# Kernel optimization log

Measured on AMD Instinct MI355X. Metric: run time of the kernel, lower is better.

## Reference

```python
import jax, jax.numpy as jnp
import numpy as np

KERNEL = 5
STRIDE = 1
DN = ('NHWC', 'HWIO', 'NHWC')
PRIOR_VAR = 0.01


def setup_inputs() -> dict:
    key = jax.random.key(0)
    k1, k2, k3 = jax.random.split(key, 3)
    mu_in = jax.random.normal(k1, (32, 224, 224, 3), dtype=jnp.float32)
    # GlorotNormal-ish scale for a 5x5x3 -> 64 kernel
    w_mu = jax.random.normal(k2, (5, 5, 3, 64), dtype=jnp.float32) * 0.12
    # original init: uniform in [min_sigma, ini_sigma] = [-4.6, -2.25]
    w_sigma = jax.random.uniform(k3, (64,), dtype=jnp.float32, minval=-4.6, maxval=-2.25)
    return {"mu_in": mu_in, "w_mu": w_mu, "w_sigma": w_sigma}


def reference(mu_in, w_mu, w_sigma):
    # KL regularizer: broadcast of (64,) logvar against (5,5,3,64) mu, mean over all
    kl = 0.5 * jnp.mean(
        jnp.log(PRIOR_VAR) - 1.0 - w_sigma
        + jax.nn.softplus(w_sigma) / PRIOR_VAR
        + jnp.square(w_mu) / PRIOR_VAR
    )

    w_sigma_2 = jax.nn.softplus(w_sigma)  # log(1+exp(w_sigma))

    # Mean path: standard conv2d, VALID, stride 1, NHWC
    mu_out = jax.lax.conv_general_dilated(
        mu_in, w_mu, (STRIDE, STRIDE), 'VALID', dimension_numbers=DN
    )  # [B, Ho, Wo, K]

    # Variance path: per-output-location sum over the k*k*C patch of x^2 / x_dim.
    # Same math as the original extract_patches + reduce_sum, but computed as a
    # channel-summed box filter on x^2 (no im2col materialization).
    C = mu_in.shape[-1]
    x_dim = jnp.asarray(KERNEL * KERNEL * C, mu_in.dtype)
    ones_k = jnp.ones((KERNEL, KERNEL, C, 1), mu_in.dtype)
    sq = jax.lax.conv_general_dilated(
        jnp.square(mu_in), ones_k, (STRIDE, STRIDE), 'VALID', dimension_numbers=DN
    ) / x_dim  # [B, Ho, Wo, 1]

    Sigma_out = jax.nn.softplus(w_sigma_2 * sq)  # broadcast -> [B, Ho, Wo, K]
    return (mu_out, Sigma_out, kl)
```

## Files before the change

### kernel.cpp

```cpp
#include <hip/hip_runtime.h>
#include <math.h>

#define BATCH 32
#define HIN   224
#define WIN   224
#define CIN   3
#define KOUT  64
#define RK    5
#define HOUT  220
#define WOUT  220

#define TS     16
#define PATCH  20
#define SROWS  24
#define NTOT ((size_t)BATCH * HOUT * WOUT * KOUT)

typedef float  v4f    __attribute__((ext_vector_type(4)));
typedef short  short8 __attribute__((ext_vector_type(8)));

#define WS_WF_FRAGS 768
#define WS_WSG_OFF  12288

__device__ __forceinline__ float exp2_hw(float x) { float r; asm("v_exp_f32 %0, %1" : "=v"(r) : "v"(x)); return r; }
__device__ __forceinline__ float log2_hw(float x) { float r; asm("v_log_f32 %0, %1" : "=v"(r) : "v"(x)); return r; }
#define LOG2E 1.44269504088896f
#define LN2   0.69314718055995f

__device__ __forceinline__ float softplus_hw(float x) {
    float t = exp2_hw(-fabsf(x) * LOG2E);
    return fmaxf(x, 0.0f) + LN2 * log2_hw(1.0f + t);
}
__device__ __forceinline__ float softplus_pos(float y) {
    return y + LN2 * log2_hw(1.0f + exp2_hw(-y * LOG2E));
}
__device__ __forceinline__ short f2bf(float x) {
    unsigned u = __float_as_uint(x);
    u = (u + 0x7FFFu + ((u >> 16) & 1u)) >> 16;
    return (short)u;
}

__global__ __launch_bounds__(256) void vdp_prep_kernel(
    const float* __restrict__ w_mu, const float* __restrict__ w_sigma, void* __restrict__ ws)
{
    short8* wf = (short8*)ws;
    float* wsg = (float*)((char*)ws + WS_WSG_OFF);
    const int t = threadIdx.x;
    for (int f = t; f < WS_WF_FRAGS; f += 256) {
        const int s  = f >> 8;
        const int nb = (f >> 6) & 3;
        const int l  = f & 63;
        const int ch = nb * 16 + (l & 15);
        const int h2 = l >> 4;
        short8 r;
        #pragma unroll
        for (int i = 0; i < 8; ++i) {
            const int k = s * 32 + h2 * 8 + i;
            const int kh = k >> 4, inner = k & 15;
            float v = 0.0f;
            if (inner < 15 && k < 80) {
                const int kw = inner / 3;
                const int c  = inner - kw * 3;
                v = w_mu[((kh * 5 + kw) * 3 + c) * KOUT + ch];
            }
            r[i] = f2bf(v);
        }
        wf[f] = r;
    }
    if (t < KOUT) wsg[t] = softplus_hw(w_sigma[t]);
}

__global__ __launch_bounds__(256, 4) void vdp_conv_kernel(
    const float* __restrict__ mu_in, const void* __restrict__ ws, float* __restrict__ out)
{
    __shared__ float s_row[SROWS][64];
    __shared__ float s_ssq[PATCH][PATCH];
    __shared__ float s_sq[TS * TS];

    const int tid  = threadIdx.x;
    const int lane = tid & 63;
    const int wid  = tid >> 6;
    const int p    = lane & 15;
    const int h2   = lane >> 4;

    const int b = blockIdx.z;
    int ho0 = blockIdx.y * TS; if (ho0 > HOUT - TS) ho0 = HOUT - TS;
    int wo0 = blockIdx.x * TS; if (wo0 > WOUT - TS) wo0 = WOUT - TS;

    const short8* wfg = (const short8*)ws;
    short8 wf[12];
    #pragma unroll
    for (int f = 0; f < 12; ++f) wf[f] = wfg[f * 64 + lane];
    const float* wsg_g = (const float*)((const char*)ws + WS_WSG_OFF);
    const v4f wsg_kg = *(const v4f*)(wsg_g + p * 4);

    for (int idx = tid; idx < SROWS * 64; idx += 256) {
        const int r = idx >> 6, c = idx & 63;
        int rg = ho0 + r; if (rg > HIN - 1) rg = HIN - 1;
        float v = 0.0f;
        if (c < 60) v = mu_in[(((size_t)b * HIN + rg) * WIN + wo0) * CIN + c];
        s_row[r][c] = v;
    }
    __syncthreads();

    for (int idx = tid; idx < PATCH * PATCH; idx += 256) {
        const int r = idx / PATCH;
        const int px = idx - r * PATCH;
        const float x0 = s_row[r][3 * px], x1 = s_row[r][3 * px + 1], x2 = s_row[r][3 * px + 2];
        s_ssq[r][px] = fmaf(x0, x0, fmaf(x1, x1, x2 * x2));
    }
    __syncthreads();

    {
        const int pr = tid >> 4, pc = tid & 15;
        float acc = 0.0f;
        #pragma unroll
        for (int kh = 0; kh < RK; ++kh)
            #pragma unroll
            for (int kw = 0; kw < RK; ++kw)
                acc += s_ssq[pr + kh][pc + kw];
        s_sq[tid] = acc * (1.0f / 75.0f);
    }
    __syncthreads();

    #pragma unroll 1
    for (int j = 0; j < 4; ++j) {
        const int rt = (wid << 2) | j;
        const size_t rowbase = (((size_t)b * HOUT + ho0 + rt) * WOUT + wo0) * KOUT;

        short8 pf[3];
        #pragma unroll
        for (int s = 0; s < 3; ++s) {
            const float* rp = &s_row[rt + 2 * s + (h2 >> 1)][3 * p + 8 * (h2 & 1)];
            short8 r;
            #pragma unroll
            for (int i = 0; i < 8; ++i) r[i] = f2bf(rp[i]);
            pf[s] = r;
        }

        v4f acc[4];
        #pragma unroll
        for (int nb = 0; nb < 4; ++nb) {
            v4f a = {0.0f, 0.0f, 0.0f, 0.0f};
            #pragma unroll
            for (int s = 0; s < 3; ++s)
                a = __builtin_amdgcn_mfma_f32_16x16x32_bf16(wf[s * 4 + nb], pf[s], a, 0, 0, 0);
            acc[nb] = a;
        }

        float* mp = out + rowbase + (size_t)p * KOUT + h2 * 4;
        #pragma unroll
        for (int nb = 0; nb < 4; ++nb)
            *(v4f*)(mp + nb * 16) = acc[nb];

        float* sp = out + NTOT + rowbase + p * 4;
        #pragma unroll
        for (int pp = 0; pp < 4; ++pp) {
            const int px = (h2 << 2) | pp;
            const float sq = s_sq[(rt << 4) | px];
            v4f sg;
            sg.x = softplus_pos(wsg_kg.x * sq);
            sg.y = softplus_pos(wsg_kg.y * sq);
            sg.z = softplus_pos(wsg_kg.z * sq);
            sg.w = softplus_pos(wsg_kg.w * sq);
            *(v4f*)(sp + (size_t)px * KOUT) = sg;
        }
    }
}

__global__ __launch_bounds__(256) void vdp_kl_kernel(
    const float* __restrict__ w_mu,
    const float* __restrict__ w_sigma,
    float* __restrict__ out)
{
    __shared__ float red[4];
    const int tid = threadIdx.x;

    float s = 0.0f;
    for (int i = tid; i < RK * RK * CIN * KOUT; i += 256) {
        const float v = w_mu[i];
        s = fmaf(v, v, s);
    }
    float u = s * (100.0f / 4800.0f);
    if (tid < KOUT) {
        const float ws = w_sigma[tid];
        u += (-ws + softplus_hw(ws) * 100.0f) * (1.0f / 64.0f);
    }
    #pragma unroll
    for (int off = 32; off > 0; off >>= 1)
        u += __shfl_down(u, off, 64);
    if ((tid & 63) == 0) red[tid >> 6] = u;
    __syncthreads();
    if (tid == 0) {
        const float U = red[0] + red[1] + red[2] + red[3];
        out[2 * NTOT] = 0.5f * (-4.6051701860f - 1.0f + U);
    }
}

extern "C" void kernel_launch(void* const* d_in, const int* in_sizes, int n_in,
                              void* d_out, int out_size, void* d_ws, size_t ws_size,
                              hipStream_t stream)
{
    (void)in_sizes; (void)n_in; (void)ws_size; (void)out_size;
    const float* mu_in   = (const float*)d_in[0];
    const float* w_mu    = (const float*)d_in[1];
    const float* w_sigma = (const float*)d_in[2];
    float* out = (float*)d_out;

    vdp_prep_kernel<<<1, 256, 0, stream>>>(w_mu, w_sigma, d_ws);
    dim3 grid((WOUT + TS - 1) / TS, (HOUT + TS - 1) / TS, BATCH);
    vdp_conv_kernel<<<grid, 256, 0, stream>>>(mu_in, d_ws, out);
    vdp_kl_kernel<<<1, 256, 0, stream>>>(w_mu, w_sigma, out);
}
```

Before: 191.5 us.

## Retile conv to 4x32 output strips and fold KL into prep kernel

```diff
diff --git a/kernel.cpp b/kernel.cpp
--- a/kernel.cpp
+++ b/kernel.cpp
@@ -10,9 +10,6 @@
 #define HOUT  220
 #define WOUT  220
 
-#define TS     16
-#define PATCH  20
-#define SROWS  24
 #define NTOT ((size_t)BATCH * HOUT * WOUT * KOUT)
 
 typedef float  v4f    __attribute__((ext_vector_type(4)));
@@ -40,11 +37,14 @@
 }
 
 __global__ __launch_bounds__(256) void vdp_prep_kernel(
-    const float* __restrict__ w_mu, const float* __restrict__ w_sigma, void* __restrict__ ws)
+    const float* __restrict__ w_mu, const float* __restrict__ w_sigma,
+    void* __restrict__ ws, float* __restrict__ out)
 {
+    __shared__ float red[4];
     short8* wf = (short8*)ws;
     float* wsg = (float*)((char*)ws + WS_WSG_OFF);
     const int t = threadIdx.x;
+
     for (int f = t; f < WS_WF_FRAGS; f += 256) {
         const int s  = f >> 8;
         const int nb = (f >> 6) & 3;
@@ -67,14 +67,34 @@
         wf[f] = r;
     }
     if (t < KOUT) wsg[t] = softplus_hw(w_sigma[t]);
+
+    float s = 0.0f;
+    for (int i = t; i < RK * RK * CIN * KOUT; i += 256) {
+        const float v = w_mu[i];
+        s = fmaf(v, v, s);
+    }
+    float u = s * (100.0f / 4800.0f);
+    if (t < KOUT) {
+        const float wsv = w_sigma[t];
+        u += (-wsv + softplus_hw(wsv) * 100.0f) * (1.0f / 64.0f);
+    }
+    #pragma unroll
+    for (int off = 32; off > 0; off >>= 1)
+        u += __shfl_down(u, off, 64);
+    if ((t & 63) == 0) red[t >> 6] = u;
+    __syncthreads();
+    if (t == 0) {
+        const float U = red[0] + red[1] + red[2] + red[3];
+        out[2 * NTOT] = 0.5f * (-4.6051701860f - 1.0f + U);
+    }
 }
 
 __global__ __launch_bounds__(256, 4) void vdp_conv_kernel(
     const float* __restrict__ mu_in, const void* __restrict__ ws, float* __restrict__ out)
 {
-    __shared__ float s_row[SROWS][64];
-    __shared__ float s_ssq[PATCH][PATCH];
-    __shared__ float s_sq[TS * TS];
+    __shared__ float s_row[8][112];
+    __shared__ float s_ssq[8][40];
+    __shared__ float s_sq[4][32];
 
     const int tid  = threadIdx.x;
     const int lane = tid & 63;
@@ -82,9 +102,9 @@
     const int p    = lane & 15;
     const int h2   = lane >> 4;
 
-    const int b = blockIdx.z;
-    int ho0 = blockIdx.y * TS; if (ho0 > HOUT - TS) ho0 = HOUT - TS;
-    int wo0 = blockIdx.x * TS; if (wo0 > WOUT - TS) wo0 = WOUT - TS;
+    const int b  = blockIdx.z;
+    const int r0 = blockIdx.y * 4;
+    const int x0 = blockIdx.x * 32;
 
     const short8* wfg = (const short8*)ws;
     short8 wf[12];
@@ -93,50 +113,49 @@
     const float* wsg_g = (const float*)((const char*)ws + WS_WSG_OFF);
     const v4f wsg_kg = *(const v4f*)(wsg_g + p * 4);
 
-    for (int idx = tid; idx < SROWS * 64; idx += 256) {
-        const int r = idx >> 6, c = idx & 63;
-        int rg = ho0 + r; if (rg > HIN - 1) rg = HIN - 1;
-        float v = 0.0f;
-        if (c < 60) v = mu_in[(((size_t)b * HIN + rg) * WIN + wo0) * CIN + c];
-        s_row[r][c] = v;
-    }
-    __syncthreads();
-
-    for (int idx = tid; idx < PATCH * PATCH; idx += 256) {
-        const int r = idx / PATCH;
-        const int px = idx - r * PATCH;
-        const float x0 = s_row[r][3 * px], x1 = s_row[r][3 * px + 1], x2 = s_row[r][3 * px + 2];
-        s_ssq[r][px] = fmaf(x0, x0, fmaf(x1, x1, x2 * x2));
-    }
-    __syncthreads();
-
-    {
-        const int pr = tid >> 4, pc = tid & 15;
-        float acc = 0.0f;
+    const size_t inbase = ((size_t)b * HIN + r0) * (WIN * CIN);
+    for (int idx = tid; idx < 8 * 112; idx += 256) {
+        const int r = idx / 112, c = idx - r * 112;
+        int f = x0 * 3 + c; if (f > WIN * CIN - 1) f = WIN * CIN - 1;
+        s_row[r][c] = mu_in[inbase + (size_t)r * (WIN * CIN) + f];
+    }
+    __syncthreads();
+
+    for (int idx = tid; idx < 8 * 36; idx += 256) {
+        const int r = idx / 36, px = idx - r * 36;
+        const float a0 = s_row[r][3 * px], a1 = s_row[r][3 * px + 1], a2 = s_row[r][3 * px + 2];
+        s_ssq[r][px] = fmaf(a0, a0, fmaf(a1, a1, a2 * a2));
+    }
+    __syncthreads();
+
+    if (tid < 128) {
+        const int orow = tid >> 5, pc = tid & 31;
+        float a = 0.0f;
         #pragma unroll
         for (int kh = 0; kh < RK; ++kh)
             #pragma unroll
             for (int kw = 0; kw < RK; ++kw)
-                acc += s_ssq[pr + kh][pc + kw];
-        s_sq[tid] = acc * (1.0f / 75.0f);
-    }
-    __syncthreads();
-
-    #pragma unroll 1
-    for (int j = 0; j < 4; ++j) {
-        const int rt = (wid << 2) | j;
-        const size_t rowbase = (((size_t)b * HOUT + ho0 + rt) * WOUT + wo0) * KOUT;
-
+                a += s_ssq[orow + kh][pc + kw];
+        s_sq[orow][pc] = a * (1.0f / 75.0f);
+    }
+    __syncthreads();
+
+    const int rt = wid;
+    const size_t rowbase = (((size_t)b * HOUT + r0 + rt) * WOUT + x0) * KOUT;
+
+    #pragma unroll
+    for (int g = 0; g < 2; ++g) {
         short8 pf[3];
         #pragma unroll
         for (int s = 0; s < 3; ++s) {
-            const float* rp = &s_row[rt + 2 * s + (h2 >> 1)][3 * p + 8 * (h2 & 1)];
+            int ridx = rt + 2 * s + (h2 >> 1);
+            ridx = ridx > 7 ? 7 : ridx;
+            const float* rp = &s_row[ridx][3 * (16 * g + p) + 8 * (h2 & 1)];
             short8 r;
             #pragma unroll
             for (int i = 0; i < 8; ++i) r[i] = f2bf(rp[i]);
             pf[s] = r;
         }
-
         v4f acc[4];
         #pragma unroll
         for (int nb = 0; nb < 4; ++nb) {
@@ -146,17 +165,20 @@
                 a = __builtin_amdgcn_mfma_f32_16x16x32_bf16(wf[s * 4 + nb], pf[s], a, 0, 0, 0);
             acc[nb] = a;
         }
-
-        float* mp = out + rowbase + (size_t)p * KOUT + h2 * 4;
-        #pragma unroll
-        for (int nb = 0; nb < 4; ++nb)
-            *(v4f*)(mp + nb * 16) = acc[nb];
-
-        float* sp = out + NTOT + rowbase + p * 4;
-        #pragma unroll
-        for (int pp = 0; pp < 4; ++pp) {
-            const int px = (h2 << 2) | pp;
-            const float sq = s_sq[(rt << 4) | px];
+        if (x0 + 16 * g + p < WOUT) {
+            float* mp = out + rowbase + (size_t)(16 * g + p) * KOUT + h2 * 4;
+            #pragma unroll
+            for (int nb = 0; nb < 4; ++nb)
+                *(v4f*)(mp + nb * 16) = acc[nb];
+        }
+    }
+
+    float* sp = out + NTOT + rowbase + p * 4;
+    #pragma unroll
+    for (int q = 0; q < 8; ++q) {
+        const int px = 4 * q + h2;
+        if (x0 + px < WOUT) {
+            const float sq = s_sq[rt][px];
             v4f sg;
             sg.x = softplus_pos(wsg_kg.x * sq);
             sg.y = softplus_pos(wsg_kg.y * sq);
@@ -164,35 +186,6 @@
             sg.w = softplus_pos(wsg_kg.w * sq);
             *(v4f*)(sp + (size_t)px * KOUT) = sg;
         }
-    }
-}
-
-__global__ __launch_bounds__(256) void vdp_kl_kernel(
-    const float* __restrict__ w_mu,
-    const float* __restrict__ w_sigma,
-    float* __restrict__ out)
-{
-    __shared__ float red[4];
-    const int tid = threadIdx.x;
-
-    float s = 0.0f;
-    for (int i = tid; i < RK * RK * CIN * KOUT; i += 256) {
-        const float v = w_mu[i];
-        s = fmaf(v, v, s);
-    }
-    float u = s * (100.0f / 4800.0f);
-    if (tid < KOUT) {
-        const float ws = w_sigma[tid];
-        u += (-ws + softplus_hw(ws) * 100.0f) * (1.0f / 64.0f);
-    }
-    #pragma unroll
-    for (int off = 32; off > 0; off >>= 1)
-        u += __shfl_down(u, off, 64);
-    if ((tid & 63) == 0) red[tid >> 6] = u;
-    __syncthreads();
-    if (tid == 0) {
-        const float U = red[0] + red[1] + red[2] + red[3];
-        out[2 * NTOT] = 0.5f * (-4.6051701860f - 1.0f + U);
     }
 }
 
@@ -206,8 +199,7 @@
     const float* w_sigma = (const float*)d_in[2];
     float* out = (float*)d_out;
 
-    vdp_prep_kernel<<<1, 256, 0, stream>>>(w_mu, w_sigma, d_ws);
-    dim3 grid((WOUT + TS - 1) / TS, (HOUT + TS - 1) / TS, BATCH);
+    vdp_prep_kernel<<<1, 256, 0, stream>>>(w_mu, w_sigma, d_ws, out);
+    dim3 grid(7, HOUT / 4, BATCH);
     vdp_conv_kernel<<<grid, 256, 0, stream>>>(mu_in, d_ws, out);
-    vdp_kl_kernel<<<1, 256, 0, stream>>>(w_mu, w_sigma, out);
-}
+}
```

Result: slower. 211.4 us (+10.4%).

## Stage weight fragments in LDS, raise occupancy, fold KL into prep kernel

Applied to the files above, without the earlier changes.

```diff
diff --git a/kernel.cpp b/kernel.cpp
--- a/kernel.cpp
+++ b/kernel.cpp
@@ -12,7 +12,6 @@
 
 #define TS     16
 #define PATCH  20
-#define SROWS  24
 #define NTOT ((size_t)BATCH * HOUT * WOUT * KOUT)
 
 typedef float  v4f    __attribute__((ext_vector_type(4)));
@@ -40,11 +39,14 @@
 }
 
 __global__ __launch_bounds__(256) void vdp_prep_kernel(
-    const float* __restrict__ w_mu, const float* __restrict__ w_sigma, void* __restrict__ ws)
+    const float* __restrict__ w_mu, const float* __restrict__ w_sigma,
+    void* __restrict__ ws, float* __restrict__ out)
 {
+    __shared__ float red[4];
     short8* wf = (short8*)ws;
     float* wsg = (float*)((char*)ws + WS_WSG_OFF);
     const int t = threadIdx.x;
+
     for (int f = t; f < WS_WF_FRAGS; f += 256) {
         const int s  = f >> 8;
         const int nb = (f >> 6) & 3;
@@ -67,14 +69,35 @@
         wf[f] = r;
     }
     if (t < KOUT) wsg[t] = softplus_hw(w_sigma[t]);
-}
-
-__global__ __launch_bounds__(256, 4) void vdp_conv_kernel(
+
+    float s = 0.0f;
+    for (int i = t; i < RK * RK * CIN * KOUT; i += 256) {
+        const float v = w_mu[i];
+        s = fmaf(v, v, s);
+    }
+    float u = s * (100.0f / 4800.0f);
+    if (t < KOUT) {
+        const float wsv = w_sigma[t];
+        u += (-wsv + softplus_hw(wsv) * 100.0f) * (1.0f / 64.0f);
+    }
+    #pragma unroll
+    for (int off = 32; off > 0; off >>= 1)
+        u += __shfl_down(u, off, 64);
+    if ((t & 63) == 0) red[t >> 6] = u;
+    __syncthreads();
+    if (t == 0) {
+        const float U = red[0] + red[1] + red[2] + red[3];
+        out[2 * NTOT] = 0.5f * (-4.6051701860f - 1.0f + U);
+    }
+}
+
+__global__ __launch_bounds__(256, 6) void vdp_conv_kernel(
     const float* __restrict__ mu_in, const void* __restrict__ ws, float* __restrict__ out)
 {
-    __shared__ float s_row[SROWS][64];
-    __shared__ float s_ssq[PATCH][PATCH];
-    __shared__ float s_sq[TS * TS];
+    __shared__ float  s_row[PATCH][64];
+    __shared__ float  s_ssq[PATCH][PATCH];
+    __shared__ float  s_sq[TS * TS];
+    __shared__ short8 s_wf[WS_WF_FRAGS];
 
     const int tid  = threadIdx.x;
     const int lane = tid & 63;
@@ -87,17 +110,15 @@
     int wo0 = blockIdx.x * TS; if (wo0 > WOUT - TS) wo0 = WOUT - TS;
 
     const short8* wfg = (const short8*)ws;
-    short8 wf[12];
-    #pragma unroll
-    for (int f = 0; f < 12; ++f) wf[f] = wfg[f * 64 + lane];
+    for (int f = tid; f < WS_WF_FRAGS; f += 256) s_wf[f] = wfg[f];
+
     const float* wsg_g = (const float*)((const char*)ws + WS_WSG_OFF);
     const v4f wsg_kg = *(const v4f*)(wsg_g + p * 4);
 
-    for (int idx = tid; idx < SROWS * 64; idx += 256) {
+    for (int idx = tid; idx < PATCH * 64; idx += 256) {
         const int r = idx >> 6, c = idx & 63;
-        int rg = ho0 + r; if (rg > HIN - 1) rg = HIN - 1;
         float v = 0.0f;
-        if (c < 60) v = mu_in[(((size_t)b * HIN + rg) * WIN + wo0) * CIN + c];
+        if (c < 60) v = mu_in[(((size_t)b * HIN + ho0 + r) * WIN + wo0) * CIN + c];
         s_row[r][c] = v;
     }
     __syncthreads();
@@ -130,7 +151,9 @@
         short8 pf[3];
         #pragma unroll
         for (int s = 0; s < 3; ++s) {
-            const float* rp = &s_row[rt + 2 * s + (h2 >> 1)][3 * p + 8 * (h2 & 1)];
+            int ridx = rt + 2 * s + (h2 >> 1);
+            ridx = ridx > PATCH - 1 ? PATCH - 1 : ridx;
+            const float* rp = &s_row[ridx][3 * p + 8 * (h2 & 1)];
             short8 r;
             #pragma unroll
             for (int i = 0; i < 8; ++i) r[i] = f2bf(rp[i]);
@@ -143,7 +166,7 @@
             v4f a = {0.0f, 0.0f, 0.0f, 0.0f};
             #pragma unroll
             for (int s = 0; s < 3; ++s)
-                a = __builtin_amdgcn_mfma_f32_16x16x32_bf16(wf[s * 4 + nb], pf[s], a, 0, 0, 0);
+                a = __builtin_amdgcn_mfma_f32_16x16x32_bf16(s_wf[(s * 4 + nb) * 64 + lane], pf[s], a, 0, 0, 0);
             acc[nb] = a;
         }
 
@@ -167,35 +190,6 @@
     }
 }
 
-__global__ __launch_bounds__(256) void vdp_kl_kernel(
-    const float* __restrict__ w_mu,
-    const float* __restrict__ w_sigma,
-    float* __restrict__ out)
-{
-    __shared__ float red[4];
-    const int tid = threadIdx.x;
-
-    float s = 0.0f;
-    for (int i = tid; i < RK * RK * CIN * KOUT; i += 256) {
-        const float v = w_mu[i];
-        s = fmaf(v, v, s);
-    }
-    float u = s * (100.0f / 4800.0f);
-    if (tid < KOUT) {
-        const float ws = w_sigma[tid];
-        u += (-ws + softplus_hw(ws) * 100.0f) * (1.0f / 64.0f);
-    }
-    #pragma unroll
-    for (int off = 32; off > 0; off >>= 1)
-        u += __shfl_down(u, off, 64);
-    if ((tid & 63) == 0) red[tid >> 6] = u;
-    __syncthreads();
-    if (tid == 0) {
-        const float U = red[0] + red[1] + red[2] + red[3];
-        out[2 * NTOT] = 0.5f * (-4.6051701860f - 1.0f + U);
-    }
-}
-
 extern "C" void kernel_launch(void* const* d_in, const int* in_sizes, int n_in,
                               void* d_out, int out_size, void* d_ws, size_t ws_size,
                               hipStream_t stream)
@@ -206,8 +200,7 @@
     const float* w_sigma = (const float*)d_in[2];
     float* out = (float*)d_out;
 
-    vdp_prep_kernel<<<1, 256, 0, stream>>>(w_mu, w_sigma, d_ws);
+    vdp_prep_kernel<<<1, 256, 0, stream>>>(w_mu, w_sigma, d_ws, out);
     dim3 grid((WOUT + TS - 1) / TS, (HOUT + TS - 1) / TS, BATCH);
     vdp_conv_kernel<<<grid, 256, 0, stream>>>(mu_in, d_ws, out);
-    vdp_kl_kernel<<<1, 256, 0, stream>>>(w_mu, w_sigma, out);
-}
+}
```

New measurement: 222.8 us. 1.16x slower.
